# Kernel optimization log

Measured on AMD Instinct MI355X. Metric: run time of the kernel, lower is better.

Reference implementation:

```python
import jax, jax.numpy as jnp
import numpy as np

B, D_IN, UNITS = 16384, 4096, 4096
EPS = 1e-05

def setup_inputs() -> dict:
    key = jax.random.key(0)
    k1, k2 = jax.random.split(key)
    x = jax.random.normal(k1, (B, D_IN), dtype=jnp.float32)
    # glorot_uniform init for Dense kernel
    limit = np.sqrt(6.0 / (D_IN + UNITS)).astype(np.float32)
    W = jax.random.uniform(k2, (D_IN, UNITS), dtype=jnp.float32, minval=-limit, maxval=limit)
    b = jnp.zeros((UNITS,), dtype=jnp.float32)
    return {"x": x, "W": W, "b": b}

def reference(x, W, b):
    # L2-normalize each row (tf.norm axis=1, keepdims) with +1e-5 stabilizer
    x_norm = jnp.sqrt(jnp.sum(x * x, axis=1, keepdims=True)) + EPS  # [B,1]
    x_dir = x / x_norm                                              # [B,D]
    # dense + bias + ReLU
    return jax.nn.relu(x_dir @ W + b)                               # [B,UNITS]
```

## Files before the change

kernel.cpp:

```cpp
#include <hip/hip_runtime.h>

#define BROWS 16384
#define DIN   4096
#define NOUT  4096
#define EPSV  1e-5f
#define KT    (DIN / 64)

typedef __attribute__((ext_vector_type(8))) short short8;
typedef __attribute__((ext_vector_type(4))) float f32x4;

__device__ __forceinline__ unsigned short f32_to_bf16(float f) {
    union { float f; unsigned u; } v;
    v.f = f;
    unsigned r = (v.u + 0x7fffu + ((v.u >> 16) & 1u)) >> 16;
    return (unsigned short)r;
}

__global__ __launch_bounds__(256) void normalize_cast_kernel(
    const float* __restrict__ x, unsigned short* __restrict__ A) {
    const int row = blockIdx.x;
    const int tid = threadIdx.x;
    const float4* xr = (const float4*)(x + (size_t)row * DIN);
    float4 v[4];
    float ss = 0.f;
#pragma unroll
    for (int i = 0; i < 4; ++i) {
        v[i] = xr[tid + i * 256];
        ss += v[i].x * v[i].x + v[i].y * v[i].y + v[i].z * v[i].z + v[i].w * v[i].w;
    }
#pragma unroll
    for (int o = 32; o > 0; o >>= 1) ss += __shfl_down(ss, o);
    __shared__ float red[4];
    const int wave = tid >> 6, lane = tid & 63;
    if (lane == 0) red[wave] = ss;
    __syncthreads();
    const float inv = 1.f / (sqrtf(red[0] + red[1] + red[2] + red[3]) + EPSV);
    uint2* Ar = (uint2*)(A + (size_t)row * DIN);
#pragma unroll
    for (int i = 0; i < 4; ++i) {
        uint2 p;
        p.x = (unsigned)f32_to_bf16(v[i].x * inv) | ((unsigned)f32_to_bf16(v[i].y * inv) << 16);
        p.y = (unsigned)f32_to_bf16(v[i].z * inv) | ((unsigned)f32_to_bf16(v[i].w * inv) << 16);
        Ar[tid + i * 256] = p;
    }
}

__global__ __launch_bounds__(256) void transpose_cast_kernel(
    const float* __restrict__ W, unsigned short* __restrict__ Wt) {
    __shared__ float tile[64][65];
    const int bn = blockIdx.x * 64, bk = blockIdx.y * 64;
    const int t = threadIdx.x;
    const int lk = t >> 4, ln4 = (t & 15) * 4;
#pragma unroll
    for (int i = 0; i < 4; ++i) {
        float4 v = *(const float4*)(W + (size_t)(bk + lk + i * 16) * NOUT + bn + ln4);
        tile[lk + i * 16][ln4 + 0] = v.x;
        tile[lk + i * 16][ln4 + 1] = v.y;
        tile[lk + i * 16][ln4 + 2] = v.z;
        tile[lk + i * 16][ln4 + 3] = v.w;
    }
    __syncthreads();
    const int ln = t >> 4, lk4 = (t & 15) * 4;
#pragma unroll
    for (int i = 0; i < 4; ++i) {
        const int n = ln + i * 16;
        uint2 p;
        p.x = (unsigned)f32_to_bf16(tile[lk4 + 0][n]) | ((unsigned)f32_to_bf16(tile[lk4 + 1][n]) << 16);
        p.y = (unsigned)f32_to_bf16(tile[lk4 + 2][n]) | ((unsigned)f32_to_bf16(tile[lk4 + 3][n]) << 16);
        *(uint2*)(Wt + (size_t)(bn + n) * DIN + bk + lk4) = p;
    }
}


__device__ __forceinline__ void async_copy16(const unsigned short* g, unsigned short* l) {
    __builtin_amdgcn_global_load_lds(
        (const __attribute__((address_space(1))) unsigned int*)g,
        (__attribute__((address_space(3))) unsigned int*)l, 16, 0, 0);
}

__global__ __launch_bounds__(512, 2) void gemm_bias_relu_kernel(
    const unsigned short* __restrict__ A, const unsigned short* __restrict__ Wt,
    const float* __restrict__ bias, float* __restrict__ C) {
    __shared__ __align__(16) unsigned short As[2][256 * 64];
    __shared__ __align__(16) unsigned short Bs[2][256 * 64];

    const int tid = threadIdx.x;
    const int lane = tid & 63, wave = tid >> 6;
    const int wm = wave >> 2, wn = wave & 3;
    const int lm = lane & 15, q = lane >> 4;
    const int ko0 = (q ^ (lm >> 1)) * 8;
    const int ko1 = ko0 ^ 32;

    const int bid = (int)blockIdx.x;
    const int wg = (bid & 7) * 128 + (bid >> 3);
    const int n0 = (wg & 15) * 256;
    const int m0 = (wg >> 4) * 256;

    const int r0 = tid >> 3;
    const int g0 = (tid & 7) ^ ((r0 & 15) >> 1);
    const unsigned short* Ag = A + (size_t)(m0 + r0) * DIN + g0 * 8;
    const unsigned short* Bg = Wt + (size_t)(n0 + r0) * DIN + g0 * 8;
    const int ub = (tid & ~63) * 8;

#define STG_A(buf, half, kk) do { \
    const unsigned short* s_ = Ag + (size_t)(half) * (128 * DIN) + (kk); \
    unsigned short* d_ = &As[buf][(half) * 8192 + ub]; \
    async_copy16(s_, d_); \
    async_copy16(s_ + 64 * DIN, d_ + 4096); \
} while (0)
#define STG_B(buf, half, kk) do { \
    const unsigned short* s_ = Bg + (size_t)(half) * (128 * DIN) + (kk); \
    unsigned short* d_ = &Bs[buf][(half) * 8192 + ub]; \
    async_copy16(s_, d_); \
    async_copy16(s_ + 64 * DIN, d_ + 4096); \
} while (0)

    f32x4 acc[8][4] = {};

    STG_B(0, 0, 0);  STG_B(0, 1, 0);
    STG_A(0, 0, 0);  STG_A(0, 1, 0);
    STG_B(1, 0, 64); STG_B(1, 1, 64);
    STG_A(1, 0, 64);
    asm volatile("s_waitcnt vmcnt(6)" ::: "memory");
    __builtin_amdgcn_s_barrier();
    __builtin_amdgcn_sched_barrier(0);

#pragma unroll 2
    for (int kt = 0; kt < KT; ++kt) {
        const int cur = kt & 1;
        const int kb1 = (kt + 1 < KT ? kt + 1 : KT - 1) * 64;
        const int kb2 = (kt + 2 < KT ? kt + 2 : KT - 1) * 64;
        const unsigned short* as = As[cur];
        const unsigned short* bs = Bs[cur];

        short8 a0[8], a1[8], b0[4], b1[4];

#pragma unroll
        for (int i = 0; i < 8; ++i)
            a0[i] = *(const short8*)&as[(wm * 128 + i * 16 + lm) * 64 + ko0];
#pragma unroll
        for (int j = 0; j < 4; ++j)
            b0[j] = *(const short8*)&bs[(wn * 64 + j * 16 + lm) * 64 + ko0];
        STG_A(cur ^ 1, 1, kb1);
        __builtin_amdgcn_s_barrier();
        asm volatile("s_waitcnt lgkmcnt(0)" ::: "memory");
        __builtin_amdgcn_s_setprio(1);
#pragma unroll
        for (int i = 0; i < 4; ++i)
#pragma unroll
            for (int j = 0; j < 4; ++j)
                acc[i][j] = __builtin_amdgcn_mfma_f32_16x16x32_bf16(a0[i], b0[j], acc[i][j], 0, 0, 0);
        __builtin_amdgcn_s_setprio(0);
        __builtin_amdgcn_s_barrier();

#pragma unroll
        for (int j = 0; j < 4; ++j)
            b1[j] = *(const short8*)&bs[(wn * 64 + j * 16 + lm) * 64 + ko1];
        __builtin_amdgcn_s_barrier();
        asm volatile("s_waitcnt lgkmcnt(0)" ::: "memory");
        __builtin_amdgcn_s_setprio(1);
#pragma unroll
        for (int i = 4; i < 8; ++i)
#pragma unroll
            for (int j = 0; j < 4; ++j)
                acc[i][j] = __builtin_amdgcn_mfma_f32_16x16x32_bf16(a0[i], b0[j], acc[i][j], 0, 0, 0);
        __builtin_amdgcn_s_setprio(0);
        __builtin_amdgcn_s_barrier();

#pragma unroll
        for (int i = 0; i < 8; ++i)
            a1[i] = *(const short8*)&as[(wm * 128 + i * 16 + lm) * 64 + ko1];
        STG_B(cur, 0, kb2);
        STG_B(cur, 1, kb2);
        __builtin_amdgcn_s_barrier();
        asm volatile("s_waitcnt lgkmcnt(0)" ::: "memory");
        __builtin_amdgcn_s_setprio(1);
#pragma unroll
        for (int i = 0; i < 4; ++i)
#pragma unroll
            for (int j = 0; j < 4; ++j)
                acc[i][j] = __builtin_amdgcn_mfma_f32_16x16x32_bf16(a1[i], b1[j], acc[i][j], 0, 0, 0);
        __builtin_amdgcn_s_setprio(0);
        __builtin_amdgcn_s_barrier();

        STG_A(cur, 0, kb2);
        asm volatile("s_waitcnt vmcnt(6)" ::: "memory");
        __builtin_amdgcn_s_barrier();
        __builtin_amdgcn_s_setprio(1);
#pragma unroll
        for (int i = 4; i < 8; ++i)
#pragma unroll
            for (int j = 0; j < 4; ++j)
                acc[i][j] = __builtin_amdgcn_mfma_f32_16x16x32_bf16(a1[i], b1[j], acc[i][j], 0, 0, 0);
        __builtin_amdgcn_s_setprio(0);
        __builtin_amdgcn_s_barrier();
        __builtin_amdgcn_sched_barrier(0);
    }

    asm volatile("s_waitcnt vmcnt(0)" ::: "memory");

    float bj[4];
#pragma unroll
    for (int j = 0; j < 4; ++j) bj[j] = bias[n0 + wn * 64 + j * 16 + lm];
    const int colb = n0 + wn * 64 + lm;
    const int rowb = m0 + wm * 128 + (q << 2);
#pragma unroll
    for (int i = 0; i < 8; ++i) {
#pragma unroll
        for (int r = 0; r < 4; ++r) {
            float* cp = C + (size_t)(rowb + i * 16 + r) * NOUT + colb;
#pragma unroll
            for (int j = 0; j < 4; ++j) {
                float v = acc[i][j][r] + bj[j];
                __builtin_nontemporal_store(v > 0.f ? v : 0.f, cp + j * 16);
            }
        }
    }
#undef STG_A
#undef STG_B
}

extern "C" void kernel_launch(void* const* d_in, const int* in_sizes, int n_in,
                              void* d_out, int out_size, void* d_ws, size_t ws_size,
                              hipStream_t stream) {
    const float* x = (const float*)d_in[0];
    const float* W = (const float*)d_in[1];
    const float* b = (const float*)d_in[2];
    float* out = (float*)d_out;

    unsigned short* Abf = (unsigned short*)d_ws;
    unsigned short* Wt = Abf + (size_t)BROWS * DIN;

    normalize_cast_kernel<<<BROWS, 256, 0, stream>>>(x, Abf);
    transpose_cast_kernel<<<dim3(NOUT / 64, DIN / 64), 256, 0, stream>>>(W, Wt);
    gemm_bias_relu_kernel<<<dim3(NOUT / 256 * (BROWS / 256)), 512, 0, stream>>>(Abf, Wt, b, out);
}
```

Measured before the change: 1.055 ms.

## Reorder A/B fragment loads and async staging across MFMA phases

Splits the A fragment loads of the GEMM main loop into four smaller register groups, loaded just before the MFMA phase that uses them. The async global-to-LDS staging is reshuffled so B is prefetched one tile ahead and A two tiles ahead, the reverse of the previous order. Scheduling barriers are added between phases. The aim is to spread LDS reads and global loads more evenly across the four compute phases and lower register pressure, at the risk of new stalls or LDS hazards from the changed buffer reuse order.

```diff
diff --git a/kernel.cpp b/kernel.cpp
--- a/kernel.cpp
+++ b/kernel.cpp
@@ -117,10 +117,10 @@
 
     f32x4 acc[8][4] = {};
 
+    STG_A(0, 0, 0);  STG_A(0, 1, 0);
     STG_B(0, 0, 0);  STG_B(0, 1, 0);
-    STG_A(0, 0, 0);  STG_A(0, 1, 0);
-    STG_B(1, 0, 64); STG_B(1, 1, 64);
-    STG_A(1, 0, 64);
+    STG_A(1, 0, 64); STG_A(1, 1, 64);
+    STG_B(1, 0, 64);
     asm volatile("s_waitcnt vmcnt(6)" ::: "memory");
     __builtin_amdgcn_s_barrier();
     __builtin_amdgcn_sched_barrier(0);
@@ -133,15 +133,15 @@
         const unsigned short* as = As[cur];
         const unsigned short* bs = Bs[cur];
 
-        short8 a0[8], a1[8], b0[4], b1[4];
-
-#pragma unroll
-        for (int i = 0; i < 8; ++i)
-            a0[i] = *(const short8*)&as[(wm * 128 + i * 16 + lm) * 64 + ko0];
+        short8 aA[4], aB[4], aC[4], aD[4], b0[4], b1[4];
+
+#pragma unroll
+        for (int i = 0; i < 4; ++i)
+            aA[i] = *(const short8*)&as[(wm * 128 + i * 16 + lm) * 64 + ko0];
 #pragma unroll
         for (int j = 0; j < 4; ++j)
             b0[j] = *(const short8*)&bs[(wn * 64 + j * 16 + lm) * 64 + ko0];
-        STG_A(cur ^ 1, 1, kb1);
+        STG_B(cur ^ 1, 1, kb1);
         __builtin_amdgcn_s_barrier();
         asm volatile("s_waitcnt lgkmcnt(0)" ::: "memory");
         __builtin_amdgcn_s_setprio(1);
@@ -149,49 +149,58 @@
         for (int i = 0; i < 4; ++i)
 #pragma unroll
             for (int j = 0; j < 4; ++j)
-                acc[i][j] = __builtin_amdgcn_mfma_f32_16x16x32_bf16(a0[i], b0[j], acc[i][j], 0, 0, 0);
-        __builtin_amdgcn_s_setprio(0);
-        __builtin_amdgcn_s_barrier();
-
+                acc[i][j] = __builtin_amdgcn_mfma_f32_16x16x32_bf16(aA[i], b0[j], acc[i][j], 0, 0, 0);
+        __builtin_amdgcn_s_setprio(0);
+        __builtin_amdgcn_s_barrier();
+        __builtin_amdgcn_sched_barrier(0);
+
+#pragma unroll
+        for (int i = 0; i < 4; ++i)
+            aB[i] = *(const short8*)&as[(wm * 128 + (i + 4) * 16 + lm) * 64 + ko0];
+#pragma unroll
+        for (int i = 0; i < 4; ++i)
+            aD[i] = *(const short8*)&as[(wm * 128 + (i + 4) * 16 + lm) * 64 + ko1];
+        __builtin_amdgcn_s_barrier();
+        asm volatile("s_waitcnt lgkmcnt(0)" ::: "memory");
+        __builtin_amdgcn_s_setprio(1);
+#pragma unroll
+        for (int i = 0; i < 4; ++i)
+#pragma unroll
+            for (int j = 0; j < 4; ++j)
+                acc[4 + i][j] = __builtin_amdgcn_mfma_f32_16x16x32_bf16(aB[i], b0[j], acc[4 + i][j], 0, 0, 0);
+        __builtin_amdgcn_s_setprio(0);
+        __builtin_amdgcn_s_barrier();
+        __builtin_amdgcn_sched_barrier(0);
+
+#pragma unroll
+        for (int i = 0; i < 4; ++i)
+            aC[i] = *(const short8*)&as[(wm * 128 + i * 16 + lm) * 64 + ko1];
 #pragma unroll
         for (int j = 0; j < 4; ++j)
             b1[j] = *(const short8*)&bs[(wn * 64 + j * 16 + lm) * 64 + ko1];
+        STG_A(cur, 0, kb2);
         __builtin_amdgcn_s_barrier();
         asm volatile("s_waitcnt lgkmcnt(0)" ::: "memory");
         __builtin_amdgcn_s_setprio(1);
 #pragma unroll
-        for (int i = 4; i < 8; ++i)
-#pragma unroll
-            for (int j = 0; j < 4; ++j)
-                acc[i][j] = __builtin_amdgcn_mfma_f32_16x16x32_bf16(a0[i], b0[j], acc[i][j], 0, 0, 0);
-        __builtin_amdgcn_s_setprio(0);
-        __builtin_amdgcn_s_barrier();
-
-#pragma unroll
-        for (int i = 0; i < 8; ++i)
-            a1[i] = *(const short8*)&as[(wm * 128 + i * 16 + lm) * 64 + ko1];
+        for (int i = 0; i < 4; ++i)
+#pragma unroll
+            for (int j = 0; j < 4; ++j)
+                acc[i][j] = __builtin_amdgcn_mfma_f32_16x16x32_bf16(aC[i], b1[j], acc[i][j], 0, 0, 0);
+        __builtin_amdgcn_s_setprio(0);
+        __builtin_amdgcn_s_barrier();
+        __builtin_amdgcn_sched_barrier(0);
+
+        STG_A(cur, 1, kb2);
         STG_B(cur, 0, kb2);
-        STG_B(cur, 1, kb2);
-        __builtin_amdgcn_s_barrier();
-        asm volatile("s_waitcnt lgkmcnt(0)" ::: "memory");
-        __builtin_amdgcn_s_setprio(1);
-#pragma unroll
-        for (int i = 0; i < 4; ++i)
-#pragma unroll
-            for (int j = 0; j < 4; ++j)
-                acc[i][j] = __builtin_amdgcn_mfma_f32_16x16x32_bf16(a1[i], b1[j], acc[i][j], 0, 0, 0);
-        __builtin_amdgcn_s_setprio(0);
-        __builtin_amdgcn_s_barrier();
-
-        STG_A(cur, 0, kb2);
         asm volatile("s_waitcnt vmcnt(6)" ::: "memory");
         __builtin_amdgcn_s_barrier();
         __builtin_amdgcn_s_setprio(1);
 #pragma unroll
-        for (int i = 4; i < 8; ++i)
-#pragma unroll
-            for (int j = 0; j < 4; ++j)
-                acc[i][j] = __builtin_amdgcn_mfma_f32_16x16x32_bf16(a1[i], b1[j], acc[i][j], 0, 0, 0);
+        for (int i = 0; i < 4; ++i)
+#pragma unroll
+            for (int j = 0; j < 4; ++j)
+                acc[4 + i][j] = __builtin_amdgcn_mfma_f32_16x16x32_bf16(aD[i], b1[j], acc[4 + i][j], 0, 0, 0);
         __builtin_amdgcn_s_setprio(0);
         __builtin_amdgcn_s_barrier();
         __builtin_amdgcn_sched_barrier(0);
```

New measurement: 1.040 ms. Within noise of the previous version (-1.4%).
